# Kernel tuning notes

Hardware: AMD Instinct MI355X
Metric: run time of the kernel (lower is better)

The kernel has to match this reference:

```python
import jax, jax.numpy as jnp
import numpy as np

H = 1024   # hidden_size == memory_size
NH = 4     # num_attention_heads
HD = H // NH
M = 8192   # total memory items
B, S = 4, 2048
EPS = 1e-5


def _ln(x, g, b):
    mu = jnp.mean(x, -1, keepdims=True)
    var = jnp.mean((x - mu) ** 2, -1, keepdims=True)
    return (x - mu) / jnp.sqrt(var + EPS) * g + b


def setup_inputs() -> dict:
    key = jax.random.key(0)
    ks = jax.random.split(key, 16)
    s = 0.02
    return {
        "query_hidden": jax.random.normal(ks[0], (B, S, H), jnp.float32),
        "mem_keys": jax.random.normal(ks[1], (M, H), jnp.float32),
        "importance": jax.random.uniform(ks[2], (M,), jnp.float32),
        "recency": jax.random.uniform(ks[3], (M,), jnp.float32),
        "access_count": jax.random.uniform(ks[4], (M,), jnp.float32),
        "Wq": s * jax.random.normal(ks[5], (H, H), jnp.float32),
        "bq": jnp.zeros((H,), jnp.float32),
        "in_w": s * jax.random.normal(ks[6], (3 * H, H), jnp.float32),
        "in_b": jnp.zeros((3 * H,), jnp.float32),
        "out_w": s * jax.random.normal(ks[7], (H, H), jnp.float32),
        "out_b": jnp.zeros((H,), jnp.float32),
        "gate_w": s * jax.random.normal(ks[8], (H, 2 * H), jnp.float32),
        "gate_b": jnp.zeros((H,), jnp.float32),
        "int_w1": s * jax.random.normal(ks[9], (2 * H, 2 * H), jnp.float32),
        "int_b1": jnp.zeros((2 * H,), jnp.float32),
        "int_ln_g": jnp.ones((2 * H,), jnp.float32),
        "int_ln_b": jnp.zeros((2 * H,), jnp.float32),
        "int_w2": s * jax.random.normal(ks[10], (H, 2 * H), jnp.float32),
        "int_b2": jnp.zeros((H,), jnp.float32),
        "ln1_g": jnp.ones((H,), jnp.float32),
        "ln1_b": jnp.zeros((H,), jnp.float32),
        "ln2_g": jnp.ones((H,), jnp.float32),
        "ln2_b": jnp.zeros((H,), jnp.float32),
        "sel_params": jnp.ones((3,), jnp.float32) / 3.0,
        "top_k": 2048,
    }


def reference(query_hidden, mem_keys, importance, recency, access_count,
              Wq, bq, in_w, in_b, out_w, out_b, gate_w, gate_b,
              int_w1, int_b1, int_ln_g, int_ln_b, int_w2, int_b2,
              ln1_g, ln1_b, ln2_g, ln2_b, sel_params, top_k):
    b, s, _ = query_hidden.shape
    # HTPS selection: softmax-weighted mix of importance / recency / frequency
    w = jax.nn.softmax(sel_params)
    freq = access_count / jnp.max(access_count)
    sel = w[0] * importance + w[1] * recency + w[2] * freq
    _, idx = jax.lax.top_k(sel, top_k)
    mem = mem_keys[idx]                      # [K, H]
    mem_n = _ln(mem, ln1_g, ln1_b)           # layer_norm1 on memory

    q = query_hidden @ Wq.T + bq             # query_proj  [B,S,H]
    wq, wk, wv = in_w[:H], in_w[H:2 * H], in_w[2 * H:]
    bqi, bki, bvi = in_b[:H], in_b[H:2 * H], in_b[2 * H:]
    # Batched MHA: the per-position loop is equivalent to all S queries at once
    Q = (q @ wq.T + bqi).reshape(b, s, NH, HD)
    K = (mem_n @ wk.T + bki).reshape(top_k, NH, HD)   # shared across batch
    V = (mem_n @ wv.T + bvi).reshape(top_k, NH, HD)
    scores = jnp.einsum('bshd,khd->bhsk', Q, K) / jnp.sqrt(jnp.float32(HD))
    attn = jax.nn.softmax(scores, axis=-1)
    ctx = jnp.einsum('bhsk,khd->bshd', attn, V).reshape(b, s, H)
    attn_out = ctx @ out_w.T + out_b

    cat = jnp.concatenate([query_hidden, attn_out], axis=-1)   # [B,S,2H]
    gate = jax.nn.sigmoid(cat @ gate_w.T + gate_b)
    h1 = _ln(cat @ int_w1.T + int_b1, int_ln_g, int_ln_b)
    integ = jax.nn.gelu(h1, approximate=False) @ int_w2.T + int_b2
    return _ln(query_hidden + gate * integ, ln2_g, ln2_b)
```

## Files before the change

kernel.cpp:

```cpp
#include <hip/hip_runtime.h>

#define HDIM 1024
#define MMEM 8192
#define TOPK 2048
#define NROWS 8192
#define LNEPS 1e-5f

typedef unsigned short ushort_t;
typedef __bf16 bf16x8 __attribute__((ext_vector_type(8)));
typedef float f32x4 __attribute__((ext_vector_type(4)));
typedef __attribute__((address_space(1))) const void GVoid;
typedef __attribute__((address_space(3))) void LVoid;

__device__ __forceinline__ ushort_t f2bf(float f) {
    union { float f; unsigned u; } c; c.f = f;
    unsigned r = c.u + 0x7fffu + ((c.u >> 16) & 1u);
    return (ushort_t)(r >> 16);
}
__device__ __forceinline__ float bf2f(ushort_t u) {
    union { unsigned u; float f; } c; c.u = ((unsigned)u) << 16; return c.f;
}
__device__ __forceinline__ float blk_red(float v, int op, float* red) {
    #pragma unroll
    for (int o = 32; o; o >>= 1) {
        float u = __shfl_down(v, o);
        v = op ? fmaxf(v, u) : v + u;
    }
    if ((threadIdx.x & 63) == 0) red[threadIdx.x >> 6] = v;
    __syncthreads();
    float r = op ? fmaxf(fmaxf(red[0], red[1]), fmaxf(red[2], red[3]))
                 : (red[0] + red[1]) + (red[2] + red[3]);
    __syncthreads();
    return r;
}

__global__ __launch_bounds__(256) void sel_prep(const float* __restrict__ sp,
        const float* __restrict__ imp, const float* __restrict__ rec,
        const float* __restrict__ ac, float* __restrict__ sel) {
    __shared__ float red[4];
    float p0 = sp[0], p1 = sp[1], p2 = sp[2];
    float mx = fmaxf(p0, fmaxf(p1, p2));
    float e0 = expf(p0 - mx), e1 = expf(p1 - mx), e2 = expf(p2 - mx);
    float inv = 1.f / (e0 + e1 + e2);
    float w0 = e0 * inv, w1 = e1 * inv, w2 = e2 * inv;
    float m = -1e30f;
    for (int i = threadIdx.x; i < MMEM; i += 256) m = fmaxf(m, ac[i]);
    m = blk_red(m, 1, red);
    float rinv = 1.f / m;
    for (int i = threadIdx.x; i < MMEM; i += 256)
        sel[i] = w0 * imp[i] + w1 * rec[i] + w2 * (ac[i] * rinv);
}

__global__ __launch_bounds__(256) void topk_rank(const float* __restrict__ sel,
                                                 int* __restrict__ idx) {
    __shared__ float s[MMEM];
    __shared__ int pc[256];
    for (int t = threadIdx.x; t < MMEM / 4; t += 256)
        reinterpret_cast<float4*>(s)[t] = reinterpret_cast<const float4*>(sel)[t];
    __syncthreads();
    const int li = threadIdx.x & 31;
    const int jc = threadIdx.x >> 5;
    const int i  = blockIdx.x * 32 + li;
    const float si = s[i];
    int cnt = 0;
    const float4* sv = reinterpret_cast<const float4*>(s) + jc * 256;
    #pragma unroll 4
    for (int t = 0; t < 256; ++t) {
        float4 v = sv[t];
        int j0 = jc * 1024 + t * 4;
        cnt += (v.x > si) || (v.x == si && (j0 + 0) < i);
        cnt += (v.y > si) || (v.y == si && (j0 + 1) < i);
        cnt += (v.z > si) || (v.z == si && (j0 + 2) < i);
        cnt += (v.w > si) || (v.w == si && (j0 + 3) < i);
    }
    pc[threadIdx.x] = cnt;
    __syncthreads();
    if (threadIdx.x < 32) {
        int r = 0;
        #pragma unroll
        for (int c = 0; c < 8; ++c) r += pc[c * 32 + threadIdx.x];
        if (r < TOPK) idx[r] = blockIdx.x * 32 + threadIdx.x;
    }
}

__global__ __launch_bounds__(256) void gather_ln(const float* __restrict__ mem_keys,
        const int* __restrict__ idx, const float* __restrict__ g,
        const float* __restrict__ b, ushort_t* __restrict__ out) {
    __shared__ float red[4];
    int src = idx[blockIdx.x] & (MMEM - 1);
    const float* x = mem_keys + (size_t)src * HDIM;
    float4 v = reinterpret_cast<const float4*>(x)[threadIdx.x];
    float s = v.x + v.y + v.z + v.w;
    float ss = v.x*v.x + v.y*v.y + v.z*v.z + v.w*v.w;
    s  = blk_red(s, 0, red);
    ss = blk_red(ss, 0, red);
    float mu = s * (1.f / HDIM);
    float var = ss * (1.f / HDIM) - mu * mu;
    float rstd = rsqrtf(var + LNEPS);
    int c = threadIdx.x * 4;
    ushort4 o;
    o.x = f2bf((v.x - mu) * rstd * g[c+0] + b[c+0]);
    o.y = f2bf((v.y - mu) * rstd * g[c+1] + b[c+1]);
    o.z = f2bf((v.z - mu) * rstd * g[c+2] + b[c+2]);
    o.w = f2bf((v.w - mu) * rstd * g[c+3] + b[c+3]);
    *reinterpret_cast<ushort4*>(out + (size_t)blockIdx.x * HDIM + c) = o;
}

__global__ __launch_bounds__(256) void cvt_bf16(const float* __restrict__ in,
                                                ushort_t* __restrict__ out) {
    size_t i = ((size_t)blockIdx.x * 256 + threadIdx.x) * 4;
    float4 v = *reinterpret_cast<const float4*>(in + i);
    ushort4 o = { f2bf(v.x), f2bf(v.y), f2bf(v.z), f2bf(v.w) };
    *reinterpret_cast<ushort4*>(out + i) = o;
}

__global__ __launch_bounds__(256) void cvt_x_cat(const float* __restrict__ x,
                                                 ushort_t* __restrict__ cat) {
    size_t i = ((size_t)blockIdx.x * 256 + threadIdx.x) * 4;
    size_t row = i >> 10, col = i & 1023;
    float4 v = *reinterpret_cast<const float4*>(x + i);
    ushort4 o = { f2bf(v.x), f2bf(v.y), f2bf(v.z), f2bf(v.w) };
    *reinterpret_cast<ushort4*>(cat + row * 2048 + col) = o;
}

__global__ __launch_bounds__(256) void softmax_rows(ushort_t* __restrict__ sc) {
    __shared__ float red[4];
    ushort_t* p = sc + (size_t)blockIdx.x * 2048 + threadIdx.x * 8;
    ushort4 a = reinterpret_cast<const ushort4*>(p)[0];
    ushort4 bq = reinterpret_cast<const ushort4*>(p)[1];
    float v[8] = { bf2f(a.x), bf2f(a.y), bf2f(a.z), bf2f(a.w),
                   bf2f(bq.x), bf2f(bq.y), bf2f(bq.z), bf2f(bq.w) };
    float mx = v[0];
    #pragma unroll
    for (int j = 1; j < 8; ++j) mx = fmaxf(mx, v[j]);
    mx = blk_red(mx, 1, red);
    float s = 0.f;
    #pragma unroll
    for (int j = 0; j < 8; ++j) { v[j] = expf(v[j] - mx); s += v[j]; }
    s = blk_red(s, 0, red);
    float inv = 1.f / s;
    ushort4 o1 = { f2bf(v[0]*inv), f2bf(v[1]*inv), f2bf(v[2]*inv), f2bf(v[3]*inv) };
    ushort4 o2 = { f2bf(v[4]*inv), f2bf(v[5]*inv), f2bf(v[6]*inv), f2bf(v[7]*inv) };
    reinterpret_cast<ushort4*>(p)[0] = o1;
    reinterpret_cast<ushort4*>(p)[1] = o2;
}

__global__ __launch_bounds__(256) void ln_gelu(ushort_t* h1,
        const float* __restrict__ g, const float* __restrict__ b) {
    __shared__ float red[4];
    ushort_t* p = h1 + (size_t)blockIdx.x * 2048 + threadIdx.x * 8;
    ushort4 a = reinterpret_cast<const ushort4*>(p)[0];
    ushort4 c = reinterpret_cast<const ushort4*>(p)[1];
    float v[8] = { bf2f(a.x), bf2f(a.y), bf2f(a.z), bf2f(a.w),
                   bf2f(c.x), bf2f(c.y), bf2f(c.z), bf2f(c.w) };
    float s = 0.f, ss = 0.f;
    #pragma unroll
    for (int j = 0; j < 8; ++j) { s += v[j]; ss += v[j]*v[j]; }
    s  = blk_red(s, 0, red);
    ss = blk_red(ss, 0, red);
    float mu = s * (1.f / 2048.f);
    float var = ss * (1.f / 2048.f) - mu * mu;
    float rstd = rsqrtf(var + LNEPS);
    int c0 = threadIdx.x * 8;
    ushort_t o[8];
    #pragma unroll
    for (int j = 0; j < 8; ++j) {
        float xn = (v[j] - mu) * rstd * g[c0 + j] + b[c0 + j];
        float ge = 0.5f * xn * (1.f + erff(xn * 0.70710678118654752f));
        o[j] = f2bf(ge);
    }
    ushort4 o1 = { o[0], o[1], o[2], o[3] };
    ushort4 o2 = { o[4], o[5], o[6], o[7] };
    reinterpret_cast<ushort4*>(p)[0] = o1;
    reinterpret_cast<ushort4*>(p)[1] = o2;
}

__global__ __launch_bounds__(256) void final_ln(const float* __restrict__ x,
        const float* gate, const ushort_t* __restrict__ integ,
        const float* __restrict__ g, const float* __restrict__ b,
        float* out) {
    __shared__ float red[4];
    size_t base = (size_t)blockIdx.x * HDIM + threadIdx.x * 4;
    float4 xv = *reinterpret_cast<const float4*>(x + base);
    float4 gv = *reinterpret_cast<const float4*>(gate + base);
    ushort4 iv = *reinterpret_cast<const ushort4*>(integ + base);
    float v[4] = { xv.x + gv.x*bf2f(iv.x), xv.y + gv.y*bf2f(iv.y),
                   xv.z + gv.z*bf2f(iv.z), xv.w + gv.w*bf2f(iv.w) };
    float s = v[0]+v[1]+v[2]+v[3];
    float ss = v[0]*v[0]+v[1]*v[1]+v[2]*v[2]+v[3]*v[3];
    s  = blk_red(s, 0, red);
    ss = blk_red(ss, 0, red);
    float mu = s * (1.f / HDIM);
    float var = ss * (1.f / HDIM) - mu * mu;
    float rstd = rsqrtf(var + LNEPS);
    int c = threadIdx.x * 4;
    float4 o;
    o.x = (v[0] - mu) * rstd * g[c+0] + b[c+0];
    o.y = (v[1] - mu) * rstd * g[c+1] + b[c+1];
    o.z = (v[2] - mu) * rstd * g[c+2] + b[c+2];
    o.w = (v[3] - mu) * rstd * g[c+3] + b[c+3];
    *reinterpret_cast<float4*>(out + base) = o;
}

template<int EPI, int BIAS>
__global__ __launch_bounds__(256, 2)
void gemm_bt(const ushort_t* __restrict__ A, const ushort_t* __restrict__ B,
             const float* __restrict__ bias, void* __restrict__ Cv,
             int K, int lda, int ldb, int ldc,
             long long sA1, long long sA2, long long sAz,
             long long sB1, long long sB2, long long sBz,
             long long sC1, long long sC2, long long sCz,
             int z2n, int zbase, float scale)
{
    __shared__ __align__(16) ushort_t As[8192];
    __shared__ __align__(16) ushort_t Bs[8192];
    const int zz = blockIdx.z;
    const int zg = zz + zbase;
    const int z1 = zg / z2n, z2 = zg - z1 * z2n;
    A += (size_t)(z1 * sA1 + z2 * sA2 + zz * sAz);
    B += (size_t)(z1 * sB1 + z2 * sB2 + zz * sBz);
    const size_t cOff = (size_t)(z1 * sC1 + z2 * sC2 + zz * sCz);
    const int m0 = blockIdx.y * 128, n0 = blockIdx.x * 128;
    const int tid = threadIdx.x;
    const int w = tid >> 6, l = tid & 63;
    const int wm = w >> 1, wn = w & 1;

    f32x4 acc[4][4] = {};

    const int srow = l >> 3;
    const int scol = ((l & 7) ^ srow) << 3;

    for (int k0 = 0; k0 < K; k0 += 64) {
        #pragma unroll
        for (int i = 0; i < 4; ++i) {
            const int c = i * 4 + w;
            const int row = c * 8 + srow;
            const ushort_t* ga = A + (size_t)(m0 + row) * lda + (k0 + scol);
            const ushort_t* gb = B + (size_t)(n0 + row) * ldb + (k0 + scol);
            __builtin_amdgcn_global_load_lds((GVoid*)ga, (LVoid*)(As + c * 512), 16, 0, 0);
            __builtin_amdgcn_global_load_lds((GVoid*)gb, (LVoid*)(Bs + c * 512), 16, 0, 0);
        }
        __syncthreads();
        #pragma unroll
        for (int kk = 0; kk < 2; ++kk) {
            bf16x8 af[4], bfv[4];
            #pragma unroll
            for (int m = 0; m < 4; ++m) {
                const int row = wm * 64 + m * 16 + (l & 15);
                const int cb = ((kk * 64) + ((l >> 4) * 16)) ^ ((row & 7) << 4);
                af[m] = *reinterpret_cast<const bf16x8*>(
                    reinterpret_cast<const char*>(As) + row * 128 + cb);
            }
            #pragma unroll
            for (int n = 0; n < 4; ++n) {
                const int row = wn * 64 + n * 16 + (l & 15);
                const int cb = ((kk * 64) + ((l >> 4) * 16)) ^ ((row & 7) << 4);
                bfv[n] = *reinterpret_cast<const bf16x8*>(
                    reinterpret_cast<const char*>(Bs) + row * 128 + cb);
            }
            #pragma unroll
            for (int m = 0; m < 4; ++m)
                #pragma unroll
                for (int n = 0; n < 4; ++n)
                    acc[m][n] = __builtin_amdgcn_mfma_f32_16x16x32_bf16(
                        af[m], bfv[n], acc[m][n], 0, 0, 0);
        }
        __syncthreads();
    }

    #pragma unroll
    for (int m = 0; m < 4; ++m) {
        const int grow = m0 + wm * 64 + m * 16 + ((l >> 4) << 2);
        #pragma unroll
        for (int n = 0; n < 4; ++n) {
            const int gcol = n0 + wn * 64 + n * 16 + (l & 15);
            float bc = (BIAS == 1) ? bias[gcol] : 0.f;
            #pragma unroll
            for (int j = 0; j < 4; ++j) {
                float v = acc[m][n][j] * scale;
                if (BIAS == 1) v += bc;
                if (BIAS == 2) v += bias[grow + j];
                if (EPI == 2) v = 1.f / (1.f + expf(-v));
                const size_t off = cOff + (size_t)(grow + j) * ldc + gcol;
                if (EPI == 1) ((ushort_t*)Cv)[off] = f2bf(v);
                else          ((float*)Cv)[off]    = v;
            }
        }
    }
}

extern "C" void kernel_launch(void* const* d_in, const int* in_sizes, int n_in,
                              void* d_out, int out_size, void* d_ws, size_t ws_size,
                              hipStream_t stream) {
    const float* x          = (const float*)d_in[0];
    const float* mem_keys   = (const float*)d_in[1];
    const float* importance = (const float*)d_in[2];
    const float* recency    = (const float*)d_in[3];
    const float* access_cnt = (const float*)d_in[4];
    const float* Wq         = (const float*)d_in[5];
    const float* bq         = (const float*)d_in[6];
    const float* in_w       = (const float*)d_in[7];
    const float* in_b       = (const float*)d_in[8];
    const float* out_w      = (const float*)d_in[9];
    const float* out_b      = (const float*)d_in[10];
    const float* gate_w     = (const float*)d_in[11];
    const float* gate_b     = (const float*)d_in[12];
    const float* int_w1     = (const float*)d_in[13];
    const float* int_b1     = (const float*)d_in[14];
    const float* int_ln_g   = (const float*)d_in[15];
    const float* int_ln_b   = (const float*)d_in[16];
    const float* int_w2     = (const float*)d_in[17];
    const float* int_b2     = (const float*)d_in[18];
    const float* ln1_g      = (const float*)d_in[19];
    const float* ln1_b      = (const float*)d_in[20];
    const float* ln2_g      = (const float*)d_in[21];
    const float* ln2_b      = (const float*)d_in[22];
    const float* sel_params = (const float*)d_in[23];

    char* ws = (char*)d_ws;
    size_t off = 0;
    auto alloc = [&](size_t bytes) -> char* {
        char* p = ws + off;
        off = (off + bytes + 255) & ~(size_t)255;
        return p;
    };

    float*    sel      = (float*)alloc(MMEM * 4);
    int*      idx      = (int*)alloc(TOPK * 4);
    ushort_t* wq_bf    = (ushort_t*)alloc((size_t)1048576 * 2);
    ushort_t* inw_bf   = (ushort_t*)alloc((size_t)3145728 * 2);
    ushort_t* outw_bf  = (ushort_t*)alloc((size_t)1048576 * 2);
    ushort_t* gatew_bf = (ushort_t*)alloc((size_t)2097152 * 2);
    ushort_t* intw1_bf = (ushort_t*)alloc((size_t)4194304 * 2);
    ushort_t* intw2_bf = (ushort_t*)alloc((size_t)2097152 * 2);
    ushort_t* mem_n    = (ushort_t*)alloc((size_t)TOPK * HDIM * 2);
    ushort_t* Kbuf     = (ushort_t*)alloc((size_t)TOPK * HDIM * 2);
    ushort_t* Vt       = (ushort_t*)alloc((size_t)HDIM * TOPK * 2);
    ushort_t* cat      = (ushort_t*)alloc((size_t)NROWS * 2048 * 2);
    ushort_t* qQ       = (ushort_t*)alloc((size_t)NROWS * 2048 * 2);
    ushort_t* qbuf     = qQ;
    ushort_t* Qbuf     = qQ + (size_t)NROWS * HDIM;
    ushort_t* h1       = qQ;
    ushort_t* ctx      = (ushort_t*)alloc((size_t)NROWS * HDIM * 2);
    ushort_t* integ    = ctx;
    float*    gatev    = (float*)d_out;

    int NC = 8;
    while (NC > 1 && off + (size_t)NC * 8388608 > ws_size) NC >>= 1;
    ushort_t* scores = (ushort_t*)alloc((size_t)NC * 8388608);

    cvt_bf16<<<1024, 256, 0, stream>>>(Wq, wq_bf);
    cvt_bf16<<<3072, 256, 0, stream>>>(in_w, inw_bf);
    cvt_bf16<<<1024, 256, 0, stream>>>(out_w, outw_bf);
    cvt_bf16<<<2048, 256, 0, stream>>>(gate_w, gatew_bf);
    cvt_bf16<<<4096, 256, 0, stream>>>(int_w1, intw1_bf);
    cvt_bf16<<<2048, 256, 0, stream>>>(int_w2, intw2_bf);
    cvt_x_cat<<<8192, 256, 0, stream>>>(x, cat);

    sel_prep<<<1, 256, 0, stream>>>(sel_params, importance, recency, access_cnt, sel);
    topk_rank<<<MMEM/32, 256, 0, stream>>>(sel, idx);
    gather_ln<<<TOPK, 256, 0, stream>>>(mem_keys, idx, ln1_g, ln1_b, mem_n);

    gemm_bt<1,1><<<dim3(8,64,1), 256, 0, stream>>>(cat, wq_bf, bq, qbuf,
        1024, 2048, 1024, 1024, 0,0,0, 0,0,0, 0,0,0, 1, 0, 1.f);
    gemm_bt<1,1><<<dim3(8,64,1), 256, 0, stream>>>(qbuf, inw_bf, in_b, Qbuf,
        1024, 1024, 1024, 1024, 0,0,0, 0,0,0, 0,0,0, 1, 0, 1.f);
    gemm_bt<1,1><<<dim3(8,16,1), 256, 0, stream>>>(mem_n, inw_bf + 1048576, in_b + 1024,
        Kbuf, 1024, 1024, 1024, 1024, 0,0,0, 0,0,0, 0,0,0, 1, 0, 1.f);
    gemm_bt<1,2><<<dim3(16,8,1), 256, 0, stream>>>(inw_bf + 2097152, mem_n, in_b + 2048,
        Vt, 1024, 1024, 1024, 2048, 0,0,0, 0,0,0, 0,0,0, 1, 0, 1.f);

    for (int c0 = 0; c0 < 16; c0 += NC) {
        gemm_bt<1,0><<<dim3(16,16,NC), 256, 0, stream>>>(Qbuf, Kbuf, nullptr, scores,
            256, 1024, 1024, 2048,
            2097152, 256, 0,  0, 256, 0,  0, 0, 4194304, 4, c0, 0.0625f);
        softmax_rows<<<NC * 2048, 256, 0, stream>>>(scores);
        gemm_bt<1,0><<<dim3(2,16,NC), 256, 0, stream>>>(scores, Vt, nullptr, ctx,
            2048, 2048, 2048, 1024,
            0, 0, 4194304,  0, 524288, 0,  2097152, 256, 0, 4, c0, 1.f);
    }

    gemm_bt<1,1><<<dim3(8,64,1), 256, 0, stream>>>(ctx, outw_bf, out_b,
        (void*)(cat + 1024), 1024, 1024, 1024, 2048, 0,0,0, 0,0,0, 0,0,0, 1, 0, 1.f);

    gemm_bt<2,1><<<dim3(8,64,1), 256, 0, stream>>>(cat, gatew_bf, gate_b, gatev,
        2048, 2048, 2048, 1024, 0,0,0, 0,0,0, 0,0,0, 1, 0, 1.f);
    gemm_bt<1,1><<<dim3(16,64,1), 256, 0, stream>>>(cat, intw1_bf, int_b1, h1,
        2048, 2048, 2048, 2048, 0,0,0, 0,0,0, 0,0,0, 1, 0, 1.f);
    ln_gelu<<<NROWS, 256, 0, stream>>>(h1, int_ln_g, int_ln_b);
    gemm_bt<1,1><<<dim3(8,64,1), 256, 0, stream>>>(h1, intw2_bf, int_b2, integ,
        2048, 2048, 2048, 1024, 0,0,0, 0,0,0, 0,0,0, 1, 0, 1.f);
    final_ln<<<NROWS, 256, 0, stream>>>(x, gatev, integ, ln2_g, ln2_b, (float*)d_out);
}
```

Baseline: 631.6 us.

## Add 256-row double-buffered bf16 MFMA GEMM kernel and use it for large GEMMs

Adds a new gemm256 kernel with 256xBN tiles and 512 threads. It double-buffers direct global-to-LDS loads with an XOR swizzle and raises wave priority around the MFMA blocks. Most large GEMMs (projections, attention scores, attention-times-V, gate, and the integration MLP) now use it instead of the 128-tile gemm_bt. The aim is more data reuse per tile and better overlap of loads with compute. The cost is higher register and LDS pressure, and fewer blocks on some launches, which may hurt occupancy.

```diff
diff --git a/kernel.cpp b/kernel.cpp
--- a/kernel.cpp
+++ b/kernel.cpp
@@ -278,6 +278,137 @@
             #pragma unroll
             for (int j = 0; j < 4; ++j) {
                 float v = acc[m][n][j] * scale;
+                if (BIAS == 1) v += bc;
+                if (BIAS == 2) v += bias[grow + j];
+                if (EPI == 2) v = 1.f / (1.f + expf(-v));
+                const size_t off = cOff + (size_t)(grow + j) * ldc + gcol;
+                if (EPI == 1) ((ushort_t*)Cv)[off] = f2bf(v);
+                else          ((float*)Cv)[off]    = v;
+            }
+        }
+    }
+}
+
+template<int BN, int EPI, int BIAS>
+__global__ __launch_bounds__(512, 2)
+void gemm256(const ushort_t* __restrict__ A, const ushort_t* __restrict__ B,
+             const float* __restrict__ bias, void* __restrict__ Cv,
+             int K, int lda, int ldb, int ldc,
+             long long sA1, long long sA2, long long sAz,
+             long long sB1, long long sB2, long long sBz,
+             long long sC1, long long sC2, long long sCz,
+             int z2n, int zbase, float scale)
+{
+    constexpr int NF   = BN / 64;
+    constexpr int LB   = BN / 64;
+    constexpr int LTOT = 4 + LB;
+    __shared__ __align__(16) ushort_t As[2][256 * 64];
+    __shared__ __align__(16) ushort_t Bs[2][BN * 64];
+
+    const int zz = blockIdx.z;
+    const int zg = zz + zbase;
+    const int z1 = zg / z2n, z2 = zg - z1 * z2n;
+    A += (size_t)(z1 * sA1 + z2 * sA2 + zz * sAz);
+    B += (size_t)(z1 * sB1 + z2 * sB2 + zz * sBz);
+    const size_t cOff = (size_t)(z1 * sC1 + z2 * sC2 + zz * sCz);
+
+    const int m0 = blockIdx.y * 256, n0 = blockIdx.x * BN;
+    const int tid = threadIdx.x;
+    const int wid = tid >> 6, l = tid & 63;
+    const int wm = wid >> 2, wn = wid & 3;
+    const int NT = K >> 6;
+
+    const int srow8 = l >> 3;
+    const int scol  = ((l & 7) ^ srow8) << 3;
+
+    auto STAGE = [&](int t, int p) {
+        const int k0 = t << 6;
+        #pragma unroll
+        for (int j = 0; j < 4; ++j) {
+            const int c = j * 8 + wid;
+            const int row = c * 8 + srow8;
+            const ushort_t* ga = A + (size_t)(m0 + row) * lda + (k0 + scol);
+            __builtin_amdgcn_global_load_lds((GVoid*)ga, (LVoid*)(&As[p][0] + c * 512), 16, 0, 0);
+        }
+        #pragma unroll
+        for (int j = 0; j < LB; ++j) {
+            const int c = j * 8 + wid;
+            const int row = c * 8 + srow8;
+            const ushort_t* gb = B + (size_t)(n0 + row) * ldb + (k0 + scol);
+            __builtin_amdgcn_global_load_lds((GVoid*)gb, (LVoid*)(&Bs[p][0] + c * 512), 16, 0, 0);
+        }
+    };
+
+    f32x4 acc[8][NF] = {};
+
+    STAGE(0, 0);
+    STAGE(1, 1);
+    asm volatile("s_waitcnt vmcnt(%0)" :: "i"(LTOT) : "memory");
+    __builtin_amdgcn_s_barrier();
+    __builtin_amdgcn_sched_barrier(0);
+
+    for (int t = 0; t < NT; ++t) {
+        const int p = t & 1;
+        const char* Ab = reinterpret_cast<const char*>(&As[p][0]);
+        const char* Bb = reinterpret_cast<const char*>(&Bs[p][0]);
+
+        bf16x8 bfv[NF][2];
+        #pragma unroll
+        for (int n = 0; n < NF; ++n)
+            #pragma unroll
+            for (int kk = 0; kk < 2; ++kk) {
+                const int row = wn * (BN / 4) + n * 16 + (l & 15);
+                const int cb = ((kk * 64) + ((l >> 4) * 16)) ^ ((row & 7) << 4);
+                bfv[n][kk] = *reinterpret_cast<const bf16x8*>(Bb + row * 128 + cb);
+            }
+        #pragma unroll
+        for (int mq = 0; mq < 2; ++mq) {
+            bf16x8 af[4][2];
+            #pragma unroll
+            for (int m = 0; m < 4; ++m)
+                #pragma unroll
+                for (int kk = 0; kk < 2; ++kk) {
+                    const int row = wm * 128 + (mq * 4 + m) * 16 + (l & 15);
+                    const int cb = ((kk * 64) + ((l >> 4) * 16)) ^ ((row & 7) << 4);
+                    af[m][kk] = *reinterpret_cast<const bf16x8*>(Ab + row * 128 + cb);
+                }
+            __builtin_amdgcn_s_setprio(1);
+            #pragma unroll
+            for (int m = 0; m < 4; ++m)
+                #pragma unroll
+                for (int n = 0; n < NF; ++n)
+                    #pragma unroll
+                    for (int kk = 0; kk < 2; ++kk)
+                        acc[mq * 4 + m][n] = __builtin_amdgcn_mfma_f32_16x16x32_bf16(
+                            af[m][kk], bfv[n][kk], acc[mq * 4 + m][n], 0, 0, 0);
+            __builtin_amdgcn_s_setprio(0);
+        }
+
+        asm volatile("s_waitcnt lgkmcnt(0)" ::: "memory");
+        __builtin_amdgcn_s_barrier();
+        __builtin_amdgcn_sched_barrier(0);
+        if (t + 2 < NT) {
+            STAGE(t + 2, p);
+            asm volatile("s_waitcnt vmcnt(%0)" :: "i"(LTOT) : "memory");
+            __builtin_amdgcn_s_barrier();
+            __builtin_amdgcn_sched_barrier(0);
+        } else if (t + 2 == NT) {
+            asm volatile("s_waitcnt vmcnt(0)" ::: "memory");
+            __builtin_amdgcn_s_barrier();
+            __builtin_amdgcn_sched_barrier(0);
+        }
+    }
+
+    #pragma unroll
+    for (int mi = 0; mi < 8; ++mi) {
+        const int grow = m0 + wm * 128 + mi * 16 + ((l >> 4) << 2);
+        #pragma unroll
+        for (int n = 0; n < NF; ++n) {
+            const int gcol = n0 + wn * (BN / 4) + n * 16 + (l & 15);
+            float bc = (BIAS == 1) ? bias[gcol] : 0.f;
+            #pragma unroll
+            for (int j = 0; j < 4; ++j) {
+                float v = acc[mi][n][j] * scale;
                 if (BIAS == 1) v += bc;
                 if (BIAS == 2) v += bias[grow + j];
                 if (EPI == 2) v = 1.f / (1.f + expf(-v));
@@ -361,9 +492,9 @@
     topk_rank<<<MMEM/32, 256, 0, stream>>>(sel, idx);
     gather_ln<<<TOPK, 256, 0, stream>>>(mem_keys, idx, ln1_g, ln1_b, mem_n);
 
-    gemm_bt<1,1><<<dim3(8,64,1), 256, 0, stream>>>(cat, wq_bf, bq, qbuf,
+    gemm256<128,1,1><<<dim3(8,32,1), 512, 0, stream>>>(cat, wq_bf, bq, qbuf,
         1024, 2048, 1024, 1024, 0,0,0, 0,0,0, 0,0,0, 1, 0, 1.f);
-    gemm_bt<1,1><<<dim3(8,64,1), 256, 0, stream>>>(qbuf, inw_bf, in_b, Qbuf,
+    gemm256<128,1,1><<<dim3(8,32,1), 512, 0, stream>>>(qbuf, inw_bf, in_b, Qbuf,
         1024, 1024, 1024, 1024, 0,0,0, 0,0,0, 0,0,0, 1, 0, 1.f);
     gemm_bt<1,1><<<dim3(8,16,1), 256, 0, stream>>>(mem_n, inw_bf + 1048576, in_b + 1024,
         Kbuf, 1024, 1024, 1024, 1024, 0,0,0, 0,0,0, 0,0,0, 1, 0, 1.f);
@@ -371,24 +502,24 @@
         Vt, 1024, 1024, 1024, 2048, 0,0,0, 0,0,0, 0,0,0, 1, 0, 1.f);
 
     for (int c0 = 0; c0 < 16; c0 += NC) {
-        gemm_bt<1,0><<<dim3(16,16,NC), 256, 0, stream>>>(Qbuf, Kbuf, nullptr, scores,
+        gemm256<256,1,0><<<dim3(8,8,NC), 512, 0, stream>>>(Qbuf, Kbuf, nullptr, scores,
             256, 1024, 1024, 2048,
             2097152, 256, 0,  0, 256, 0,  0, 0, 4194304, 4, c0, 0.0625f);
         softmax_rows<<<NC * 2048, 256, 0, stream>>>(scores);
-        gemm_bt<1,0><<<dim3(2,16,NC), 256, 0, stream>>>(scores, Vt, nullptr, ctx,
+        gemm256<128,1,0><<<dim3(2,8,NC), 512, 0, stream>>>(scores, Vt, nullptr, ctx,
             2048, 2048, 2048, 1024,
             0, 0, 4194304,  0, 524288, 0,  2097152, 256, 0, 4, c0, 1.f);
     }
 
-    gemm_bt<1,1><<<dim3(8,64,1), 256, 0, stream>>>(ctx, outw_bf, out_b,
+    gemm256<128,1,1><<<dim3(8,32,1), 512, 0, stream>>>(ctx, outw_bf, out_b,
         (void*)(cat + 1024), 1024, 1024, 1024, 2048, 0,0,0, 0,0,0, 0,0,0, 1, 0, 1.f);
 
-    gemm_bt<2,1><<<dim3(8,64,1), 256, 0, stream>>>(cat, gatew_bf, gate_b, gatev,
+    gemm256<128,2,1><<<dim3(8,32,1), 512, 0, stream>>>(cat, gatew_bf, gate_b, gatev,
         2048, 2048, 2048, 1024, 0,0,0, 0,0,0, 0,0,0, 1, 0, 1.f);
-    gemm_bt<1,1><<<dim3(16,64,1), 256, 0, stream>>>(cat, intw1_bf, int_b1, h1,
+    gemm256<256,1,1><<<dim3(8,32,1), 512, 0, stream>>>(cat, intw1_bf, int_b1, h1,
         2048, 2048, 2048, 2048, 0,0,0, 0,0,0, 0,0,0, 1, 0, 1.f);
     ln_gelu<<<NROWS, 256, 0, stream>>>(h1, int_ln_g, int_ln_b);
-    gemm_bt<1,1><<<dim3(8,64,1), 256, 0, stream>>>(h1, intw2_bf, int_b2, integ,
+    gemm256<128,1,1><<<dim3(8,32,1), 512, 0, stream>>>(h1, intw2_bf, int_b2, integ,
         2048, 2048, 2048, 1024, 0,0,0, 0,0,0, 0,0,0, 1, 0, 1.f);
     final_ln<<<NROWS, 256, 0, stream>>>(x, gatev, integ, ln2_g, ln2_b, (float*)d_out);
 }
```

Result: slower. 714.4 us (+13.1%).

## Add 256x256 eight-wave pipelined GEMM for scores and int_w1 projections

Applied to the files above, without the earlier changes.

Adds a new GEMM kernel with 256x256 output tiles, 512 threads, double-buffered LDS and a fine-grained schedule. It interleaves asynchronous global-to-LDS loads of the next K tiles with MFMA compute on quarter-tiles, using explicit vmcnt waits, barriers and setprio. The attention scores GEMM and the int_w1 GEMM now use it instead of the 128x128 kernel, aiming to raise data reuse and hide memory latency. The cost is 128KB of LDS per block and heavy register use, which limits occupancy, plus hand-tuned barrier ordering that is easy to get wrong.

```diff
diff --git a/kernel.cpp b/kernel.cpp
--- a/kernel.cpp
+++ b/kernel.cpp
@@ -226,7 +226,6 @@
     const int wm = w >> 1, wn = w & 1;
 
     f32x4 acc[4][4] = {};
-
     const int srow = l >> 3;
     const int scol = ((l & 7) ^ srow) << 3;
 
@@ -289,6 +288,137 @@
     }
 }
 
+#define SBAR8 asm volatile("s_barrier" ::: "memory")
+#define VM6   asm volatile("s_waitcnt vmcnt(6)" ::: "memory")
+#define VM0   asm volatile("s_waitcnt vmcnt(0)" ::: "memory")
+
+#define STG8(P, ISB, H, T) do {                                               \
+    const int k0_ = (T) << 6;                                                 \
+    ushort_t* L_ = (ISB) ? &Bs[P][0] : &As[P][0];                             \
+    const ushort_t* G_ = (ISB) ? B : A;                                       \
+    const int ld_ = (ISB) ? ldb : lda;                                        \
+    const int b0_ = (ISB) ? n0 : m0;                                          \
+    _Pragma("unroll")                                                         \
+    for (int j_ = 0; j_ < 2; ++j_) {                                          \
+        const int c_ = j_ * 8 + wid;                                          \
+        const int r_ = (H) * 128 + c_ * 8 + srow8;                            \
+        const ushort_t* g_ = G_ + (size_t)(b0_ + r_) * ld_ + (k0_ + scol);    \
+        __builtin_amdgcn_global_load_lds((GVoid*)g_,                          \
+            (LVoid*)(L_ + ((H) * 16 + c_) * 512), 16, 0, 0);                  \
+    }                                                                         \
+} while (0)
+
+#define COMP8(P, MQ, NQ) do {                                                 \
+    const char* Ab_ = reinterpret_cast<const char*>(&As[P][0]);               \
+    const char* Bb_ = reinterpret_cast<const char*>(&Bs[P][0]);               \
+    bf16x8 af_[4][2], bf_[2][2];                                              \
+    _Pragma("unroll")                                                         \
+    for (int m_ = 0; m_ < 4; ++m_)                                            \
+        _Pragma("unroll")                                                     \
+        for (int kk_ = 0; kk_ < 2; ++kk_) {                                   \
+            const int row_ = (MQ) * 128 + wm * 64 + m_ * 16 + (l & 15);       \
+            const int cb_ = ((kk_ * 64) + ((l >> 4) * 16)) ^ ((row_ & 7) << 4); \
+            af_[m_][kk_] = *reinterpret_cast<const bf16x8*>(Ab_ + row_ * 128 + cb_); \
+        }                                                                     \
+    _Pragma("unroll")                                                         \
+    for (int n_ = 0; n_ < 2; ++n_)                                            \
+        _Pragma("unroll")                                                     \
+        for (int kk_ = 0; kk_ < 2; ++kk_) {                                   \
+            const int col_ = (NQ) * 128 + wn * 32 + n_ * 16 + (l & 15);       \
+            const int cb_ = ((kk_ * 64) + ((l >> 4) * 16)) ^ ((col_ & 7) << 4); \
+            bf_[n_][kk_] = *reinterpret_cast<const bf16x8*>(Bb_ + col_ * 128 + cb_); \
+        }                                                                     \
+    __builtin_amdgcn_s_setprio(1);                                            \
+    _Pragma("unroll")                                                         \
+    for (int m_ = 0; m_ < 4; ++m_)                                            \
+        _Pragma("unroll")                                                     \
+        for (int n_ = 0; n_ < 2; ++n_)                                        \
+            _Pragma("unroll")                                                 \
+            for (int kk_ = 0; kk_ < 2; ++kk_)                                 \
+                acc[(MQ)*4 + m_][(NQ)*2 + n_] =                               \
+                    __builtin_amdgcn_mfma_f32_16x16x32_bf16(                  \
+                        af_[m_][kk_], bf_[n_][kk_],                           \
+                        acc[(MQ)*4 + m_][(NQ)*2 + n_], 0, 0, 0);              \
+    __builtin_amdgcn_s_setprio(0);                                            \
+} while (0)
+
+template<int EPI, int BIAS>
+__global__ __launch_bounds__(512, 2)
+void gemm8p(const ushort_t* __restrict__ A, const ushort_t* __restrict__ B,
+            const float* __restrict__ bias, void* __restrict__ Cv,
+            int K, int lda, int ldb, int ldc,
+            long long sA1, long long sA2, long long sBz2, long long sCz,
+            int z2n, int zbase, float scale)
+{
+    __shared__ __align__(16) ushort_t As[2][16384];
+    __shared__ __align__(16) ushort_t Bs[2][16384];
+
+    const int zz = blockIdx.z;
+    const int zg = zz + zbase;
+    const int z1 = zg / z2n, z2 = zg - z1 * z2n;
+    A += (size_t)(z1 * sA1 + z2 * sA2);
+    B += (size_t)(z2 * sBz2);
+    const size_t cOff = (size_t)zz * sCz;
+
+    const int m0 = blockIdx.y * 256, n0 = blockIdx.x * 256;
+    const int tid = threadIdx.x;
+    const int wid = tid >> 6, l = tid & 63;
+    const int wm = wid >> 2, wn = wid & 3;
+    const int srow8 = l >> 3;
+    const int scol  = ((l & 7) ^ srow8) << 3;
+
+    f32x4 acc[8][4] = {};
+
+    const int NT = K >> 6;
+    const int jlast = (NT >> 1) - 1;
+
+    STG8(0, 0, 0, 0); STG8(0, 1, 0, 0);
+    STG8(0, 0, 1, 0); STG8(0, 1, 1, 0);
+    STG8(1, 0, 0, 1); STG8(1, 1, 0, 1);
+
+    for (int j = 0; j <= jlast; ++j) {
+        const int ta = 2 * j, tb = 2 * j + 1;
+        STG8(1, 1, 1, tb);
+        VM6; SBAR8;
+        COMP8(0, 0, 0); SBAR8;
+        STG8(1, 0, 1, tb);
+        COMP8(0, 1, 0); SBAR8;
+        if (j < jlast) STG8(0, 1, 0, ta + 2);
+        COMP8(0, 0, 1); SBAR8;
+        if (j < jlast) STG8(0, 0, 0, ta + 2);
+        COMP8(0, 1, 1); SBAR8;
+        if (j < jlast) { STG8(0, 1, 1, ta + 2); VM6; }
+        else          { VM0; }
+        SBAR8;
+        COMP8(1, 0, 0); SBAR8;
+        if (j < jlast) STG8(0, 0, 1, ta + 2);
+        COMP8(1, 1, 0); SBAR8;
+        if (j < jlast) STG8(1, 1, 0, tb + 2);
+        COMP8(1, 0, 1); SBAR8;
+        if (j < jlast) STG8(1, 0, 0, tb + 2);
+        COMP8(1, 1, 1); SBAR8;
+    }
+
+    #pragma unroll
+    for (int mi = 0; mi < 8; ++mi) {
+        const int grow = m0 + (mi >> 2) * 128 + wm * 64 + (mi & 3) * 16 + ((l >> 4) << 2);
+        #pragma unroll
+        for (int ni = 0; ni < 4; ++ni) {
+            const int gcol = n0 + (ni >> 1) * 128 + wn * 32 + (ni & 1) * 16 + (l & 15);
+            float bc = (BIAS == 1) ? bias[gcol] : 0.f;
+            #pragma unroll
+            for (int j = 0; j < 4; ++j) {
+                float v = acc[mi][ni][j] * scale;
+                if (BIAS == 1) v += bc;
+                if (EPI == 2) v = 1.f / (1.f + expf(-v));
+                const size_t off = cOff + (size_t)(grow + j) * ldc + gcol;
+                if (EPI == 1) ((ushort_t*)Cv)[off] = f2bf(v);
+                else          ((float*)Cv)[off]    = v;
+            }
+        }
+    }
+}
+
 extern "C" void kernel_launch(void* const* d_in, const int* in_sizes, int n_in,
                               void* d_out, int out_size, void* d_ws, size_t ws_size,
                               hipStream_t stream) {
@@ -371,9 +501,9 @@
         Vt, 1024, 1024, 1024, 2048, 0,0,0, 0,0,0, 0,0,0, 1, 0, 1.f);
 
     for (int c0 = 0; c0 < 16; c0 += NC) {
-        gemm_bt<1,0><<<dim3(16,16,NC), 256, 0, stream>>>(Qbuf, Kbuf, nullptr, scores,
+        gemm8p<1,0><<<dim3(8,8,NC), 512, 0, stream>>>(Qbuf, Kbuf, nullptr, scores,
             256, 1024, 1024, 2048,
-            2097152, 256, 0,  0, 256, 0,  0, 0, 4194304, 4, c0, 0.0625f);
+            2097152, 256, 256, 4194304, 4, c0, 0.0625f);
         softmax_rows<<<NC * 2048, 256, 0, stream>>>(scores);
         gemm_bt<1,0><<<dim3(2,16,NC), 256, 0, stream>>>(scores, Vt, nullptr, ctx,
             2048, 2048, 2048, 1024,
@@ -385,8 +515,8 @@
 
     gemm_bt<2,1><<<dim3(8,64,1), 256, 0, stream>>>(cat, gatew_bf, gate_b, gatev,
         2048, 2048, 2048, 1024, 0,0,0, 0,0,0, 0,0,0, 1, 0, 1.f);
-    gemm_bt<1,1><<<dim3(16,64,1), 256, 0, stream>>>(cat, intw1_bf, int_b1, h1,
-        2048, 2048, 2048, 2048, 0,0,0, 0,0,0, 0,0,0, 1, 0, 1.f);
+    gemm8p<1,1><<<dim3(8,32,1), 512, 0, stream>>>(cat, intw1_bf, int_b1, h1,
+        2048, 2048, 2048, 2048, 0,0,0,0, 1, 0, 1.f);
     ln_gelu<<<NROWS, 256, 0, stream>>>(h1, int_ln_g, int_ln_b);
     gemm_bt<1,1><<<dim3(8,64,1), 256, 0, stream>>>(h1, intw2_bf, int_b2, integ,
         2048, 2048, 2048, 1024, 0,0,0, 0,0,0, 0,0,0, 1, 0, 1.f);
```

Measured after the change: 665.0 us. +5.3%, slower.

## Fold query projection into MHA Q projection and remap workgroups across XCDs

Applied to the files above, without the earlier changes.

Precomputes the combined weight Wq_in·Wq and the folded bias (Wq_in·bq + bqi), so the two chained 8192x1024x1024 GEMMs for the query become a single GEMM plus a small 1024^3 weight GEMM. Adds a transposing bf16 convert kernel for Wq and a bias-fold kernel. It also remaps workgroup IDs in gemm_bt so that consecutive tiles are grouped per XCD, aiming for better L2 locality. The weight fold is recomputed every call, and rounding the folded weight to bf16 changes numerics slightly.

```diff
diff --git a/kernel.cpp b/kernel.cpp
--- a/kernel.cpp
+++ b/kernel.cpp
@@ -114,6 +114,39 @@
     *reinterpret_cast<ushort4*>(out + i) = o;
 }
 
+__global__ __launch_bounds__(256) void cvt_t_bf16(const float* __restrict__ in,
+                                                  ushort_t* __restrict__ out) {
+    __shared__ ushort_t t[64][65];
+    const int bx = blockIdx.x * 64, by = blockIdx.y * 64;
+    const int r = threadIdx.x >> 4, c4 = (threadIdx.x & 15) << 2;
+    #pragma unroll
+    for (int rr = 0; rr < 64; rr += 16) {
+        float4 v = *reinterpret_cast<const float4*>(in + (size_t)(by + r + rr) * 1024 + bx + c4);
+        t[r + rr][c4 + 0] = f2bf(v.x);
+        t[r + rr][c4 + 1] = f2bf(v.y);
+        t[r + rr][c4 + 2] = f2bf(v.z);
+        t[r + rr][c4 + 3] = f2bf(v.w);
+    }
+    __syncthreads();
+    #pragma unroll
+    for (int rr = 0; rr < 64; rr += 16) {
+        const int i = r + rr;
+        ushort4 o = { t[c4 + 0][i], t[c4 + 1][i], t[c4 + 2][i], t[c4 + 3][i] };
+        *reinterpret_cast<ushort4*>(out + (size_t)(bx + i) * 1024 + by + c4) = o;
+    }
+}
+
+__global__ __launch_bounds__(256) void bias_fold(const float* __restrict__ wq,
+        const float* __restrict__ bq, const float* __restrict__ bqi,
+        float* __restrict__ beff) {
+    __shared__ float red[4];
+    const float4 wv = reinterpret_cast<const float4*>(wq + (size_t)blockIdx.x * 1024)[threadIdx.x];
+    const float4 bv = reinterpret_cast<const float4*>(bq)[threadIdx.x];
+    float s = wv.x*bv.x + wv.y*bv.y + wv.z*bv.z + wv.w*bv.w;
+    s = blk_red(s, 0, red);
+    if (threadIdx.x == 0) beff[blockIdx.x] = s + bqi[blockIdx.x];
+}
+
 __global__ __launch_bounds__(256) void cvt_x_cat(const float* __restrict__ x,
                                                  ushort_t* __restrict__ cat) {
     size_t i = ((size_t)blockIdx.x * 256 + threadIdx.x) * 4;
@@ -220,13 +253,19 @@
     A += (size_t)(z1 * sA1 + z2 * sA2 + zz * sAz);
     B += (size_t)(z1 * sB1 + z2 * sB2 + zz * sBz);
     const size_t cOff = (size_t)(z1 * sC1 + z2 * sC2 + zz * sCz);
-    const int m0 = blockIdx.y * 128, n0 = blockIdx.x * 128;
+
+    const int nwg = gridDim.x * gridDim.y;
+    const int wg  = blockIdx.y * gridDim.x + blockIdx.x;
+    const int q8  = nwg >> 3, r8 = nwg & 7;
+    const int xcd = wg & 7, lo = wg >> 3;
+    const int wgid = (xcd < r8 ? xcd * (q8 + 1) : r8 * (q8 + 1) + (xcd - r8) * q8) + lo;
+    const int m0 = (wgid / gridDim.x) * 128, n0 = (wgid % gridDim.x) * 128;
+
     const int tid = threadIdx.x;
     const int w = tid >> 6, l = tid & 63;
     const int wm = w >> 1, wn = w & 1;
 
     f32x4 acc[4][4] = {};
-
     const int srow = l >> 3;
     const int scol = ((l & 7) ^ srow) << 3;
 
@@ -327,7 +366,9 @@
 
     float*    sel      = (float*)alloc(MMEM * 4);
     int*      idx      = (int*)alloc(TOPK * 4);
-    ushort_t* wq_bf    = (ushort_t*)alloc((size_t)1048576 * 2);
+    float*    beff     = (float*)alloc(1024 * 4);
+    ushort_t* wqT_bf   = (ushort_t*)alloc((size_t)1048576 * 2);
+    ushort_t* weff_bf  = (ushort_t*)alloc((size_t)1048576 * 2);
     ushort_t* inw_bf   = (ushort_t*)alloc((size_t)3145728 * 2);
     ushort_t* outw_bf  = (ushort_t*)alloc((size_t)1048576 * 2);
     ushort_t* gatew_bf = (ushort_t*)alloc((size_t)2097152 * 2);
@@ -338,7 +379,6 @@
     ushort_t* Vt       = (ushort_t*)alloc((size_t)HDIM * TOPK * 2);
     ushort_t* cat      = (ushort_t*)alloc((size_t)NROWS * 2048 * 2);
     ushort_t* qQ       = (ushort_t*)alloc((size_t)NROWS * 2048 * 2);
-    ushort_t* qbuf     = qQ;
     ushort_t* Qbuf     = qQ + (size_t)NROWS * HDIM;
     ushort_t* h1       = qQ;
     ushort_t* ctx      = (ushort_t*)alloc((size_t)NROWS * HDIM * 2);
@@ -349,22 +389,24 @@
     while (NC > 1 && off + (size_t)NC * 8388608 > ws_size) NC >>= 1;
     ushort_t* scores = (ushort_t*)alloc((size_t)NC * 8388608);
 
-    cvt_bf16<<<1024, 256, 0, stream>>>(Wq, wq_bf);
+    cvt_t_bf16<<<dim3(16,16), 256, 0, stream>>>(Wq, wqT_bf);
     cvt_bf16<<<3072, 256, 0, stream>>>(in_w, inw_bf);
     cvt_bf16<<<1024, 256, 0, stream>>>(out_w, outw_bf);
     cvt_bf16<<<2048, 256, 0, stream>>>(gate_w, gatew_bf);
     cvt_bf16<<<4096, 256, 0, stream>>>(int_w1, intw1_bf);
     cvt_bf16<<<2048, 256, 0, stream>>>(int_w2, intw2_bf);
     cvt_x_cat<<<8192, 256, 0, stream>>>(x, cat);
+    bias_fold<<<1024, 256, 0, stream>>>(in_w, bq, in_b, beff);
+
+    gemm_bt<1,0><<<dim3(8,8,1), 256, 0, stream>>>(inw_bf, wqT_bf, nullptr, weff_bf,
+        1024, 1024, 1024, 1024, 0,0,0, 0,0,0, 0,0,0, 1, 0, 1.f);
 
     sel_prep<<<1, 256, 0, stream>>>(sel_params, importance, recency, access_cnt, sel);
     topk_rank<<<MMEM/32, 256, 0, stream>>>(sel, idx);
     gather_ln<<<TOPK, 256, 0, stream>>>(mem_keys, idx, ln1_g, ln1_b, mem_n);
 
-    gemm_bt<1,1><<<dim3(8,64,1), 256, 0, stream>>>(cat, wq_bf, bq, qbuf,
+    gemm_bt<1,1><<<dim3(8,64,1), 256, 0, stream>>>(cat, weff_bf, beff, Qbuf,
         1024, 2048, 1024, 1024, 0,0,0, 0,0,0, 0,0,0, 1, 0, 1.f);
-    gemm_bt<1,1><<<dim3(8,64,1), 256, 0, stream>>>(qbuf, inw_bf, in_b, Qbuf,
-        1024, 1024, 1024, 1024, 0,0,0, 0,0,0, 0,0,0, 1, 0, 1.f);
     gemm_bt<1,1><<<dim3(8,16,1), 256, 0, stream>>>(mem_n, inw_bf + 1048576, in_b + 1024,
         Kbuf, 1024, 1024, 1024, 1024, 0,0,0, 0,0,0, 0,0,0, 1, 0, 1.f);
     gemm_bt<1,2><<<dim3(16,8,1), 256, 0, stream>>>(inw_bf + 2097152, mem_n, in_b + 2048,
```

New measurement: 594.9 us. -5.8%, faster.
